# Optimization experiments

Hardware: AMD Instinct MI355X
Metric: run time of the kernel (lower is better)

## Reference

```python
import jax, jax.numpy as jnp
from jax import lax
import numpy as np

# ---- geometry constants (from metadata / module __init__) ----
NA = 1152            # rotview (number of projection angles)
ND = 736             # det_count
NP = 512             # reconstructed image size
VOX = 1.0 / 0.7      # vox_scaling
D   = VOX * 595.0    # source-to-isocenter distance
DD  = VOX * 490.6    # isocenter-to-detector distance
DU  = VOX * 1.2858   # detector pixel spacing
DSD = D + DD         # source-to-detector distance
ANGLES = np.linspace(0.0, 2.0 * np.pi, NA, endpoint=False) + np.pi / 2.0

# ---- Shepp-Logan Fourier filter (skimage/torch-radon construction) ----
PAD = max(64, int(2 ** np.ceil(np.log2(2 * ND))))  # 2048

def _shepp_logan_filter(size):
    n = np.concatenate([np.arange(1, size // 2 + 1, 2),
                        np.arange(size // 2 - 1, 0, -2)])
    f = np.zeros(size)
    f[0] = 0.25
    f[1::2] = -1.0 / (np.pi * n) ** 2
    four = 2.0 * np.real(np.fft.fft(f))            # ramp filter
    omega = np.pi * np.fft.fftfreq(size)[1:]
    four[1:] *= np.sin(omega) / omega              # Shepp-Logan window
    return four[: size // 2 + 1].astype(np.float32)  # rfft half-spectrum

FILT = jnp.asarray(_shepp_logan_filter(PAD))
COS_A = jnp.asarray(np.cos(ANGLES).astype(np.float32))
SIN_A = jnp.asarray(np.sin(ANGLES).astype(np.float32))


def _filter_sinogram(sino):
    # sino: (NA, ND). Zero-pad to PAD, filter in Fourier domain, crop.
    padded = jnp.pad(sino, ((0, 0), (0, PAD - ND)))
    spec = jnp.fft.rfft(padded, axis=-1) * FILT
    filt = jnp.fft.irfft(spec, n=PAD, axis=-1)[:, :ND]
    return filt * (np.pi / (2.0 * NA))


def _backproject(filtered):
    # Pixel-driven fan-beam (flat detector) backprojection.
    c = (NP - 1) / 2.0
    coords = jnp.arange(NP, dtype=jnp.float32) - c
    ys, xs = jnp.meshgrid(coords, coords, indexing='ij')  # (NP, NP)

    def body(acc, inp):
        cb, sb, row = inp
        pdot = xs * cb + ys * sb            # pixel coord along source dir
        pe = -xs * sb + ys * cb             # pixel coord along detector axis
        den = D - pdot                      # source->pixel depth
        u = DSD * pe / den                  # detector coordinate (mm)
        iu = u / DU + (ND - 1) / 2.0        # fractional detector index
        i0 = jnp.floor(iu)
        frac = iu - i0
        i0i = i0.astype(jnp.int32)
        valid = (i0i >= 0) & (i0i < ND - 1) & (den > 0)
        i0c = jnp.clip(i0i, 0, ND - 2)
        v = row[i0c] * (1.0 - frac) + row[i0c + 1] * frac  # linear interp
        w = (D / den) ** 2                   # fan-beam distance weighting
        return acc + jnp.where(valid, w * v, 0.0), None

    img, _ = lax.scan(body, jnp.zeros((NP, NP), jnp.float32),
                      (COS_A, SIN_A, filtered))
    return img


def setup_inputs() -> dict:
    key = jax.random.key(0)
    x = jax.random.normal(key, (1, 1, NA, ND), dtype=jnp.float32)
    return {"x": x}


def reference(x):
    sino = x[0, 0]                          # (NA, ND) after squeeze
    filtered = _filter_sinogram(sino)
    fbp = _backproject(filtered)
    # mu -> HU -> normalize to [0, 1] window
    fbp_hu = (1000.0 * ((fbp - 0.0192) / 0.0192) - (-1024.0)) / (3072.0 - (-1024.0))
    return fbp_hu[None, None]               # (1, 1, 512, 512)
```

## Files before the change

kernel.cpp:

```cpp
#include <hip/hip_runtime.h>
#include <math.h>

#ifndef M_PI
#define M_PI 3.14159265358979323846
#endif

#define NAANG 1152
#define NDET  736
#define NPIX  512
#define PADN  2048
#define NHALF 1025
#define CHUNK 2
#define AC    (NAANG / CHUNK)

#define OFF_FILTD 0
#define OFF_H     8320
#define OFF_TRIG  16512
#define OFF_FS    25728
#define OFF_PART  3417216

__global__ void filt_spec_kernel(double* __restrict__ filt_d) {
    __shared__ double red[256];
    const int m = blockIdx.x;
    const int t = threadIdx.x;
    double s = 0.0;
    for (int j = t; j < 1024; j += 256) {
        int n = (j < 512) ? (2 * j + 1) : (2047 - 2 * j);
        double fj = -1.0 / ((M_PI * n) * (M_PI * n));
        double ang = (2.0 * M_PI) * (double)m * (double)(2 * j + 1) / (double)PADN;
        s += fj * cos(ang);
    }
    red[t] = s;
    __syncthreads();
    for (int w = 128; w > 0; w >>= 1) {
        if (t < w) red[t] += red[t + w];
        __syncthreads();
    }
    if (t == 0) {
        double four = 2.0 * (0.25 + red[0]);
        if (m > 0) {
            double om = M_PI * (double)m / (double)PADN;
            four *= sin(om) / om;
        }
        filt_d[m] = four;
    }
}

__global__ void h_kernel(const double* __restrict__ filt_d, float* __restrict__ h) {
    __shared__ double red[256];
    const int k = blockIdx.x;
    const int t = threadIdx.x;
    double s = 0.0;
    for (int m = t; m <= 1024; m += 256) {
        double c;
        if (m == 0) c = 1.0;
        else if (m == 1024) c = (k & 1) ? -1.0 : 1.0;
        else c = 2.0 * cos((2.0 * M_PI) * (double)m * (double)k / (double)PADN);
        s += filt_d[m] * c;
    }
    red[t] = s;
    __syncthreads();
    for (int w = 128; w > 0; w >>= 1) {
        if (t < w) red[t] += red[t + w];
        __syncthreads();
    }
    if (t == 0)
        h[k] = (float)(red[0] / (double)PADN * (M_PI / (2.0 * (double)NAANG)));
}

__global__ void trig_kernel(float2* __restrict__ trig) {
    int a = blockIdx.x * 256 + threadIdx.x;
    if (a < NAANG) {
        double ang = 2.0 * M_PI * (double)a / (double)NAANG + M_PI / 2.0;
        trig[a] = make_float2((float)cos(ang), (float)sin(ang));
    }
}

__global__ void conv_kernel(const float* __restrict__ x,
                            const float* __restrict__ h,
                            float* __restrict__ fs) {
    __shared__ float sh2[2816];
    __shared__ float srow[NDET];
    const int row = blockIdx.x;
    const int t = threadIdx.x;
    for (int i = t; i < 2816; i += 256) sh2[i] = h[i & (PADN - 1)];
    const float4* x4 = (const float4*)(x + row * NDET);
    for (int i = t; i < NDET / 4; i += 256) ((float4*)srow)[i] = x4[i];
    __syncthreads();

    float a0 = 0.f, a1 = 0.f, a2 = 0.f;
    const int base = t + PADN;
    #pragma unroll 2
    for (int j = 0; j < NDET; j += 4) {
        float4 r4 = *(const float4*)&srow[j];
        const float* p = &sh2[base - j];
        a0 = fmaf(r4.x, p[0],   a0); a1 = fmaf(r4.x, p[256], a1); a2 = fmaf(r4.x, p[512], a2);
        a0 = fmaf(r4.y, p[-1],  a0); a1 = fmaf(r4.y, p[255], a1); a2 = fmaf(r4.y, p[511], a2);
        a0 = fmaf(r4.z, p[-2],  a0); a1 = fmaf(r4.z, p[254], a1); a2 = fmaf(r4.z, p[510], a2);
        a0 = fmaf(r4.w, p[-3],  a0); a1 = fmaf(r4.w, p[253], a1); a2 = fmaf(r4.w, p[509], a2);
    }
    fs[row * NDET + t] = a0;
    fs[row * NDET + t + 256] = a1;
    if (t + 512 < NDET) fs[row * NDET + t + 512] = a2;
}

__global__ void backproj_kernel(const float* __restrict__ fs,
                                const float2* __restrict__ trig,
                                float* __restrict__ partial) {
    __shared__ float2 st[AC];
    const int t = threadIdx.x;
    const int zc = blockIdx.z;
    const int abase = zc * AC;
    for (int i = t; i < AC; i += 256) st[i] = trig[abase + i];
    __syncthreads();

    const int ix = blockIdx.x * 256 + t;
    const int iy = blockIdx.y;
    const float xs = (float)ix - 255.5f;
    const float ys = (float)iy - 255.5f;
    const float Dg = 850.0f;
    const float K  = (float)(1085.6 / 1.2858);

    const float* rowp = fs + abase * NDET;
    float acc = 0.0f;
    for (int a = 0; a < AC; ++a, rowp += NDET) {
        float2 cs2 = st[a];
        float cb = cs2.x, sb = cs2.y;
        float pdot = fmaf(xs, cb, ys * sb);
        float pe   = fmaf(ys, cb, -(xs * sb));
        float den  = Dg - pdot;
        float r    = __builtin_amdgcn_rcpf(den);
        float iu   = fmaf(K * pe, r, 367.5f);
        float i0f  = floorf(iu);
        float frac = iu - i0f;
        int   i0   = (int)i0f;
        int   ic   = min(max(i0, 0), NDET - 2);
        float v0 = rowp[ic];
        float v1 = rowp[ic + 1];
        float v  = fmaf(frac, v1 - v0, v0);
        float dr = Dg * r;
        float w  = dr * dr;
        w = ((unsigned)i0 < (unsigned)(NDET - 1)) ? w : 0.0f;
        acc = fmaf(w, v, acc);
    }
    partial[zc * NPIX * NPIX + iy * NPIX + ix] = acc;
}

__global__ void combine_kernel(const float* __restrict__ partial,
                               float* __restrict__ out) {
    int p = blockIdx.x * 256 + threadIdx.x;
    float s = partial[p] + partial[NPIX * NPIX + p];
    out[p] = fmaf(s, (float)(1000.0 / 0.0192 / 4096.0), 0.005859375f);
}

extern "C" void kernel_launch(void* const* d_in, const int* in_sizes, int n_in,
                              void* d_out, int out_size, void* d_ws, size_t ws_size,
                              hipStream_t stream) {
    const float* x = (const float*)d_in[0];
    float* out = (float*)d_out;

    char* ws = (char*)d_ws;
    double* filt_d = (double*)(ws + OFF_FILTD);
    float*  h      = (float*)(ws + OFF_H);
    float2* trig   = (float2*)(ws + OFF_TRIG);
    float*  fs     = (float*)(ws + OFF_FS);
    float*  part   = (float*)(ws + OFF_PART);

    filt_spec_kernel<<<NHALF, 256, 0, stream>>>(filt_d);
    h_kernel<<<PADN, 256, 0, stream>>>(filt_d, h);
    trig_kernel<<<(NAANG + 255) / 256, 256, 0, stream>>>(trig);
    conv_kernel<<<NAANG, 256, 0, stream>>>(x, h, fs);
    backproj_kernel<<<dim3(NPIX / 256, NPIX, CHUNK), 256, 0, stream>>>(fs, trig, part);
    combine_kernel<<<NPIX * NPIX / 256, 256, 0, stream>>>(part, out);
}
```

Baseline: 268.6 us.

## Register-block backprojection over two rows, vectorize convolution, fold trig into h kernel

Each backprojection thread now computes two adjacent image rows and reuses the per-angle trig terms, with K folded into a precomputed float4 table. The angle range is split into up to four chunks depending on workspace size, and launch bounds are set for occupancy. The convolution kernel uses 192 threads that each produce four outputs from vector shared-memory loads, and the trig kernel is merged into h_kernel to save a launch. The changes trade more per-thread registers and larger partial buffers for fewer redundant ALU ops and launches.

```diff
diff --git a/kernel.cpp b/kernel.cpp
--- a/kernel.cpp
+++ b/kernel.cpp
@@ -10,14 +10,12 @@
 #define NPIX  512
 #define PADN  2048
 #define NHALF 1025
-#define CHUNK 2
-#define AC    (NAANG / CHUNK)
 
 #define OFF_FILTD 0
 #define OFF_H     8320
 #define OFF_TRIG  16512
-#define OFF_FS    25728
-#define OFF_PART  3417216
+#define OFF_FS    34944
+#define OFF_PART  3426432
 
 __global__ void filt_spec_kernel(double* __restrict__ filt_d) {
     __shared__ double red[256];
@@ -46,10 +44,17 @@
     }
 }
 
-__global__ void h_kernel(const double* __restrict__ filt_d, float* __restrict__ h) {
+__global__ void h_kernel(const double* __restrict__ filt_d, float* __restrict__ h,
+                         float4* __restrict__ trig) {
     __shared__ double red[256];
     const int k = blockIdx.x;
     const int t = threadIdx.x;
+    if (t == 0 && k < NAANG) {
+        double ang = 2.0 * M_PI * (double)k / (double)NAANG + M_PI / 2.0;
+        double c = cos(ang), s = sin(ang);
+        double K = 1085.6 / 1.2858;
+        trig[k] = make_float4((float)c, (float)s, (float)(K * c), (float)(K * s));
+    }
     double s = 0.0;
     for (int m = t; m <= 1024; m += 256) {
         double c;
@@ -68,14 +73,6 @@
         h[k] = (float)(red[0] / (double)PADN * (M_PI / (2.0 * (double)NAANG)));
 }
 
-__global__ void trig_kernel(float2* __restrict__ trig) {
-    int a = blockIdx.x * 256 + threadIdx.x;
-    if (a < NAANG) {
-        double ang = 2.0 * M_PI * (double)a / (double)NAANG + M_PI / 2.0;
-        trig[a] = make_float2((float)cos(ang), (float)sin(ang));
-    }
-}
-
 __global__ void conv_kernel(const float* __restrict__ x,
                             const float* __restrict__ h,
                             float* __restrict__ fs) {
@@ -83,73 +80,90 @@
     __shared__ float srow[NDET];
     const int row = blockIdx.x;
     const int t = threadIdx.x;
-    for (int i = t; i < 2816; i += 256) sh2[i] = h[i & (PADN - 1)];
+    const float4* h4 = (const float4*)h;
+    for (int i = t; i < 704; i += 192) ((float4*)sh2)[i] = h4[i & 511];
     const float4* x4 = (const float4*)(x + row * NDET);
-    for (int i = t; i < NDET / 4; i += 256) ((float4*)srow)[i] = x4[i];
+    for (int i = t; i < NDET / 4; i += 192) ((float4*)srow)[i] = x4[i];
     __syncthreads();
 
-    float a0 = 0.f, a1 = 0.f, a2 = 0.f;
-    const int base = t + PADN;
+    const int t4 = 4 * t;
+    float o0 = 0.f, o1 = 0.f, o2 = 0.f, o3 = 0.f;
     #pragma unroll 2
     for (int j = 0; j < NDET; j += 4) {
         float4 r4 = *(const float4*)&srow[j];
-        const float* p = &sh2[base - j];
-        a0 = fmaf(r4.x, p[0],   a0); a1 = fmaf(r4.x, p[256], a1); a2 = fmaf(r4.x, p[512], a2);
-        a0 = fmaf(r4.y, p[-1],  a0); a1 = fmaf(r4.y, p[255], a1); a2 = fmaf(r4.y, p[511], a2);
-        a0 = fmaf(r4.z, p[-2],  a0); a1 = fmaf(r4.z, p[254], a1); a2 = fmaf(r4.z, p[510], a2);
-        a0 = fmaf(r4.w, p[-3],  a0); a1 = fmaf(r4.w, p[253], a1); a2 = fmaf(r4.w, p[509], a2);
+        const int A = t4 + PADN - j;
+        float4 hlo = *(const float4*)&sh2[A - 4];
+        float4 hhi = *(const float4*)&sh2[A];
+        o0 = fmaf(r4.x, hhi.x, o0); o0 = fmaf(r4.y, hlo.w, o0);
+        o0 = fmaf(r4.z, hlo.z, o0); o0 = fmaf(r4.w, hlo.y, o0);
+        o1 = fmaf(r4.x, hhi.y, o1); o1 = fmaf(r4.y, hhi.x, o1);
+        o1 = fmaf(r4.z, hlo.w, o1); o1 = fmaf(r4.w, hlo.z, o1);
+        o2 = fmaf(r4.x, hhi.z, o2); o2 = fmaf(r4.y, hhi.y, o2);
+        o2 = fmaf(r4.z, hhi.x, o2); o2 = fmaf(r4.w, hlo.w, o2);
+        o3 = fmaf(r4.x, hhi.w, o3); o3 = fmaf(r4.y, hhi.z, o3);
+        o3 = fmaf(r4.z, hhi.y, o3); o3 = fmaf(r4.w, hhi.x, o3);
     }
-    fs[row * NDET + t] = a0;
-    fs[row * NDET + t + 256] = a1;
-    if (t + 512 < NDET) fs[row * NDET + t + 512] = a2;
+    if (t < NDET / 4)
+        *(float4*)&fs[row * NDET + t4] = make_float4(o0, o1, o2, o3);
 }
 
-__global__ void backproj_kernel(const float* __restrict__ fs,
-                                const float2* __restrict__ trig,
-                                float* __restrict__ partial) {
-    __shared__ float2 st[AC];
+template<int NCH>
+__global__ __launch_bounds__(256, 8)
+void backproj_kernel(const float* __restrict__ fs,
+                     const float4* __restrict__ trig,
+                     float* __restrict__ partial) {
+    constexpr int ACL = NAANG / NCH;
+    __shared__ float4 st[ACL];
     const int t = threadIdx.x;
-    const int zc = blockIdx.z;
-    const int abase = zc * AC;
-    for (int i = t; i < AC; i += 256) st[i] = trig[abase + i];
+    const int abase = blockIdx.z * ACL;
+    for (int i = t; i < ACL; i += 256) st[i] = trig[abase + i];
     __syncthreads();
 
     const int ix = blockIdx.x * 256 + t;
-    const int iy = blockIdx.y;
-    const float xs = (float)ix - 255.5f;
-    const float ys = (float)iy - 255.5f;
+    const int iy = blockIdx.y * 2;
+    const float xs  = (float)ix - 255.5f;
+    const float ys0 = (float)iy - 255.5f;
     const float Dg = 850.0f;
-    const float K  = (float)(1085.6 / 1.2858);
 
     const float* rowp = fs + abase * NDET;
-    float acc = 0.0f;
-    for (int a = 0; a < AC; ++a, rowp += NDET) {
-        float2 cs2 = st[a];
-        float cb = cs2.x, sb = cs2.y;
-        float pdot = fmaf(xs, cb, ys * sb);
-        float pe   = fmaf(ys, cb, -(xs * sb));
-        float den  = Dg - pdot;
-        float r    = __builtin_amdgcn_rcpf(den);
-        float iu   = fmaf(K * pe, r, 367.5f);
-        float i0f  = floorf(iu);
-        float frac = iu - i0f;
-        int   i0   = (int)i0f;
-        int   ic   = min(max(i0, 0), NDET - 2);
-        float v0 = rowp[ic];
-        float v1 = rowp[ic + 1];
-        float v  = fmaf(frac, v1 - v0, v0);
-        float dr = Dg * r;
-        float w  = dr * dr;
-        w = ((unsigned)i0 < (unsigned)(NDET - 1)) ? w : 0.0f;
-        acc = fmaf(w, v, acc);
+    float acc0 = 0.f, acc1 = 0.f;
+    for (int a = 0; a < ACL; ++a, rowp += NDET) {
+        float4 q = st[a];
+        float den0 = fmaf(-xs, q.x, fmaf(-ys0, q.y, Dg));
+        float kpe0 = fmaf(ys0, q.z, -(xs * q.w));
+        float den1 = den0 - q.y;
+        float kpe1 = kpe0 + q.z;
+        float r0 = __builtin_amdgcn_rcpf(den0);
+        float r1 = __builtin_amdgcn_rcpf(den1);
+        float iu0 = fmaf(kpe0, r0, 367.5f);
+        float iu1 = fmaf(kpe1, r1, 367.5f);
+        float f0 = floorf(iu0), f1 = floorf(iu1);
+        int   i0 = (int)f0,     i1 = (int)f1;
+        int   c0 = min(max(i0, 0), NDET - 2);
+        int   c1 = min(max(i1, 0), NDET - 2);
+        float fr0 = iu0 - f0,   fr1 = iu1 - f1;
+        float a0 = rowp[c0], b0 = rowp[c0 + 1];
+        float a1 = rowp[c1], b1 = rowp[c1 + 1];
+        float v0 = fmaf(fr0, b0 - a0, a0);
+        float v1 = fmaf(fr1, b1 - a1, a1);
+        float d0 = Dg * r0, d1 = Dg * r1;
+        float w0 = d0 * d0, w1 = d1 * d1;
+        w0 = ((unsigned)i0 < (unsigned)(NDET - 1)) ? w0 : 0.f;
+        w1 = ((unsigned)i1 < (unsigned)(NDET - 1)) ? w1 : 0.f;
+        acc0 = fmaf(w0, v0, acc0);
+        acc1 = fmaf(w1, v1, acc1);
     }
-    partial[zc * NPIX * NPIX + iy * NPIX + ix] = acc;
+    partial[(blockIdx.z * NPIX + iy) * NPIX + ix] = acc0;
+    partial[(blockIdx.z * NPIX + iy + 1) * NPIX + ix] = acc1;
 }
 
+template<int NCH>
 __global__ void combine_kernel(const float* __restrict__ partial,
                                float* __restrict__ out) {
     int p = blockIdx.x * 256 + threadIdx.x;
-    float s = partial[p] + partial[NPIX * NPIX + p];
+    float s = 0.f;
+    #pragma unroll
+    for (int c = 0; c < NCH; ++c) s += partial[c * NPIX * NPIX + p];
     out[p] = fmaf(s, (float)(1000.0 / 0.0192 / 4096.0), 0.005859375f);
 }
 
@@ -162,14 +176,23 @@
     char* ws = (char*)d_ws;
     double* filt_d = (double*)(ws + OFF_FILTD);
     float*  h      = (float*)(ws + OFF_H);
-    float2* trig   = (float2*)(ws + OFF_TRIG);
+    float4* trig   = (float4*)(ws + OFF_TRIG);
     float*  fs     = (float*)(ws + OFF_FS);
     float*  part   = (float*)(ws + OFF_PART);
 
     filt_spec_kernel<<<NHALF, 256, 0, stream>>>(filt_d);
-    h_kernel<<<PADN, 256, 0, stream>>>(filt_d, h);
-    trig_kernel<<<(NAANG + 255) / 256, 256, 0, stream>>>(trig);
-    conv_kernel<<<NAANG, 256, 0, stream>>>(x, h, fs);
-    backproj_kernel<<<dim3(NPIX / 256, NPIX, CHUNK), 256, 0, stream>>>(fs, trig, part);
-    combine_kernel<<<NPIX * NPIX / 256, 256, 0, stream>>>(part, out);
+    h_kernel<<<PADN, 256, 0, stream>>>(filt_d, h, trig);
+    conv_kernel<<<NAANG, 192, 0, stream>>>(x, h, fs);
+
+    const size_t pbytes = (size_t)NPIX * NPIX * 4;
+    if (ws_size >= OFF_PART + 4 * pbytes) {
+        backproj_kernel<4><<<dim3(2, 256, 4), 256, 0, stream>>>(fs, trig, part);
+        combine_kernel<4><<<NPIX * NPIX / 256, 256, 0, stream>>>(part, out);
+    } else if (ws_size >= OFF_PART + 2 * pbytes) {
+        backproj_kernel<2><<<dim3(2, 256, 2), 256, 0, stream>>>(fs, trig, part);
+        combine_kernel<2><<<NPIX * NPIX / 256, 256, 0, stream>>>(part, out);
+    } else {
+        backproj_kernel<1><<<dim3(2, 256, 1), 256, 0, stream>>>(fs, trig, part);
+        combine_kernel<1><<<NPIX * NPIX / 256, 256, 0, stream>>>(part, out);
+    }
 }
```

New measurement: 266.8 us. About the same (-0.7%).
